# Kernel tuning notes

Measured on AMD Instinct MI355X. Metric: run time of the kernel, lower is better.

The kernel has to match this reference:

```python
import jax, jax.numpy as jnp
import numpy as np

RSQRT2 = 2 ** (-0.5)
B, S, D_IN = 2, 4096, 1024
H, D_HEAD = 8, 64            # num_heads, attention_dim (per-head qk and v dim)
QK_DIM = H * D_HEAD          # 512
V_DIM = H * D_HEAD           # 512
OUT_DIM = D_IN               # 1024 (output_dim defaults to input_dim)
LN_EPS = 1e-5


def setup_inputs() -> dict:
    key = jax.random.key(0)
    ks = jax.random.split(key, 8)
    def lecun(k, fan_in, shape):
        return jax.random.normal(k, shape, dtype=jnp.float32) * (1.0 / np.sqrt(fan_in))
    return {
        "x": jax.random.normal(ks[0], (B, S, D_IN), dtype=jnp.float32),
        # weights stored [in, out] (transposed torch Linear layout)
        "W_qk": lecun(ks[1], D_IN, (D_IN, 2 * QK_DIM)),
        "b_qk": jnp.zeros((2 * QK_DIM,), jnp.float32),
        "W_v": lecun(ks[2], D_IN, (D_IN, V_DIM)),
        "b_v": jnp.zeros((V_DIM,), jnp.float32),
        "W_out": lecun(ks[3], V_DIM, (V_DIM, OUT_DIM)),
        "b_out": jnp.zeros((OUT_DIM,), jnp.float32),
        "ln_gamma": jnp.ones((OUT_DIM,), jnp.float32),
        "ln_beta": jnp.zeros((OUT_DIM,), jnp.float32),
    }


def _layernorm(y, gamma, beta):
    mu = jnp.mean(y, axis=-1, keepdims=True)
    var = jnp.mean(jnp.square(y - mu), axis=-1, keepdims=True)
    return (y - mu) * jax.lax.rsqrt(var + LN_EPS) * gamma + beta


def reference(x, W_qk, b_qk, W_v, b_v, W_out, b_out, ln_gamma, ln_beta):
    b, s, _ = x.shape
    scale = D_HEAD ** (-0.5)
    qk = x @ W_qk + b_qk                          # [b, s, 2*h*d]
    qk = qk.reshape(b, s, H, D_HEAD, 2)           # c (q/k) is fastest axis
    q, k = qk[..., 0], qk[..., 1]                 # [b, s, h, d]
    v = (x @ W_v + b_v).reshape(b, s, H, D_HEAD)  # [b, s, h, d]
    # manual multi-head attention, full O(s^2) score matrix (as in source)
    sim = jnp.einsum("bihd,bjhd->bhij", q, k) * scale
    attn = jax.nn.softmax(sim, axis=-1)           # [b, h, i, j]
    o = jnp.einsum("bhij,bjhd->bihd", attn, v)    # [b, s, h, d]
    o = o.reshape(b, s, V_DIM)                    # 'b h s d -> b s (h d)'
    y = _layernorm(o @ W_out + b_out, ln_gamma, ln_beta)
    return (y + x) * RSQRT2
```

## Files before the change

### kernel.cpp

```cpp
#include <hip/hip_runtime.h>
#include <stdint.h>

typedef short bf16x8 __attribute__((ext_vector_type(8)));
typedef float f32x4 __attribute__((ext_vector_type(4)));
typedef unsigned short ushort_t;

#define RSQRT2_F 0.70710678118654752440f
#define QSCALE_F 0.18033688011114382f

__device__ __forceinline__ ushort_t f2bf(float f) {
  union { float f; uint32_t u; } c; c.f = f;
  uint32_t u = c.u;
  uint32_t r = (u + 0x7fffu + ((u >> 16) & 1u)) >> 16;
  return (ushort_t)r;
}
__device__ __forceinline__ float bf2f(ushort_t u) {
  union { uint32_t u; float f; } c; c.u = ((uint32_t)u) << 16;
  return c.f;
}
__device__ __forceinline__ uint32_t fbits(float f) {
  union { float f; uint32_t u; } c; c.f = f; return c.u;
}

__device__ __forceinline__ void gload_lds16(const void* g, void* l) {
  __builtin_amdgcn_global_load_lds(
      (const __attribute__((address_space(1))) void*)g,
      (__attribute__((address_space(3))) void*)l, 16, 0, 0);
}

__global__ __launch_bounds__(256) void k_cvt_x(const float* __restrict__ x,
                                               ushort_t* __restrict__ xb) {
  int i = (blockIdx.x * 256 + threadIdx.x) * 4;
  float4 f = *(const float4*)(x + i);
  ushort4 o;
  o.x = f2bf(f.x); o.y = f2bf(f.y); o.z = f2bf(f.z); o.w = f2bf(f.w);
  *(ushort4*)(xb + i) = o;
}

__global__ __launch_bounds__(256) void k_build_wqkv(const float* __restrict__ Wqk,
                                                    const float* __restrict__ bqk,
                                                    const float* __restrict__ Wv,
                                                    const float* __restrict__ bv,
                                                    ushort_t* __restrict__ Wt,
                                                    float* __restrict__ biasAll) {
  int k = blockIdx.x * 256 + threadIdx.x;
  int n = blockIdx.y;
  float w, bb;
  if (n < 512)       { w = Wqk[(size_t)k * 1024 + 2 * n] * QSCALE_F;     bb = bqk[2 * n] * QSCALE_F; }
  else if (n < 1024) { w = Wqk[(size_t)k * 1024 + 2 * (n - 512) + 1];    bb = bqk[2 * (n - 512) + 1]; }
  else               { w = Wv[(size_t)k * 512 + (n - 1024)];             bb = bv[n - 1024]; }
  Wt[(size_t)n * 1024 + k] = f2bf(w);
  if (k == 0) biasAll[n] = bb;
}

__global__ __launch_bounds__(256) void k_build_wout(const float* __restrict__ Wout,
                                                    ushort_t* __restrict__ Wt) {
  int k = blockIdx.x * 256 + threadIdx.x;
  int n = blockIdx.y;
  Wt[(size_t)n * 512 + k] = f2bf(Wout[(size_t)k * 1024 + n]);
}

template <int MODE>
__global__ __launch_bounds__(256) void k_gemm_bt(
    const ushort_t* __restrict__ A, const ushort_t* __restrict__ Bt,
    const float* __restrict__ bias,
    ushort_t* __restrict__ out0, ushort_t* __restrict__ out1, ushort_t* __restrict__ out2,
    int M, int N, int K) {
  __shared__ __align__(16) ushort_t As[4][128][8];
  __shared__ __align__(16) ushort_t Bs[4][128][8];
  const int t = threadIdx.x;
  const int lane = t & 63;
  const int wave = t >> 6;
  const int m0 = blockIdx.x * 128, n0 = blockIdx.y * 128;
  const int wm = (wave >> 1) * 64, wn = (wave & 1) * 64;
  const int lg = lane >> 4, lr = lane & 15;

  const int srow = t & 127, sg = t >> 7;
  ushort_t* lA0 = &As[sg][srow][0];
  ushort_t* lA1 = &As[sg + 2][srow][0];
  ushort_t* lB0 = &Bs[sg][srow][0];
  ushort_t* lB1 = &Bs[sg + 2][srow][0];
  const ushort_t* gA = A + (size_t)(m0 + srow) * K + sg * 8;
  const ushort_t* gB = Bt + (size_t)(n0 + srow) * K + sg * 8;

  f32x4 acc[4][4] = {};

  for (int k0 = 0; k0 < K; k0 += 32) {
    __syncthreads();
    gload_lds16(gA + k0, lA0);
    gload_lds16(gA + k0 + 16, lA1);
    gload_lds16(gB + k0, lB0);
    gload_lds16(gB + k0 + 16, lB1);
    __syncthreads();
    bf16x8 af[4], bfr[4];
#pragma unroll
    for (int mi = 0; mi < 4; mi++) af[mi] = *(const bf16x8*)&As[lg][wm + mi * 16 + lr][0];
#pragma unroll
    for (int ni = 0; ni < 4; ni++) bfr[ni] = *(const bf16x8*)&Bs[lg][wn + ni * 16 + lr][0];
#pragma unroll
    for (int mi = 0; mi < 4; mi++)
#pragma unroll
      for (int ni = 0; ni < 4; ni++)
        acc[mi][ni] = __builtin_amdgcn_mfma_f32_16x16x32_bf16(af[mi], bfr[ni], acc[mi][ni], 0, 0, 0);
  }

#pragma unroll
  for (int mi = 0; mi < 4; mi++) {
    int rowb = m0 + wm + mi * 16 + (lane >> 4) * 4;
#pragma unroll
    for (int ni = 0; ni < 4; ni++) {
      int col = n0 + wn + ni * 16 + lr;
      float bc = bias[col];
#pragma unroll
      for (int reg = 0; reg < 4; reg++) {
        int row = rowb + reg;
        float v = acc[mi][ni][reg] + bc;
        if (MODE == 0) {
          if (col < 512) {
            out0[(size_t)row * 512 + col] = f2bf(v);
          } else if (col < 1024) {
            out1[(size_t)row * 512 + (col - 512)] = f2bf(v);
          } else {
            int hd = col - 1024;
            int bb = row >> 12, s = row & 4095;
            out2[((size_t)(bb << 9) + hd) * 4096 + s] = f2bf(v);
          }
        } else {
          out0[(size_t)row * 1024 + col] = f2bf(v);
        }
      }
    }
  }
}

__global__ __launch_bounds__(256, 2) void k_attn(const ushort_t* __restrict__ Qb,
                                                 const ushort_t* __restrict__ Kb,
                                                 const ushort_t* __restrict__ Vt,
                                                 ushort_t* __restrict__ O0,
                                                 ushort_t* __restrict__ O1,
                                                 float* __restrict__ lpart) {
  __shared__ __align__(16) ushort_t Ks[2][8][64][8];
  __shared__ __align__(16) ushort_t Vs[2][8][64][8];
  __shared__ __align__(16) ushort_t Pl[4][1024];
  const int S = 4096;
  const int t = threadIdx.x, lane = t & 63, wave = t >> 6;
  const int lg = lane >> 4, lr = lane & 15;

  const int bid = blockIdx.x;
  const int xcd = bid & 7, idx = bid >> 3;
  const int bh = (xcd << 1) | (idx >> 5);
  const int rem = idx & 31;
  const int qb = rem >> 1;
  const int half = rem & 1;
  const int b = bh >> 3, h = bh & 7;
  const int qbase = qb * 256 + wave * 64;
  const int kvbase = half * 2048;

  bf16x8 qf[4][2];
#pragma unroll
  for (int su = 0; su < 4; su++) {
    const ushort_t* qp = Qb + ((size_t)(b * S + qbase + su * 16 + lr)) * 512 + h * 64 + lg * 8;
    qf[su][0] = *(const bf16x8*)qp;
    qf[su][1] = *(const bf16x8*)(qp + 32);
  }

  const int cj = t & 63, cg = t >> 6;
  const ushort_t* gK = Kb + ((size_t)b * S + cj) * 512 + h * 64 + cg * 8;
  const ushort_t* gV = Vt + ((size_t)bh * 64 + cj) * 4096 + cg * 8;

  const bf16x8 vones = {(short)0x3F80, (short)0x3F80, (short)0x3F80, (short)0x3F80,
                        (short)0x3F80, (short)0x3F80, (short)0x3F80, (short)0x3F80};

  int poff[4], pread[2];
#pragma unroll
  for (int nt = 0; nt < 4; nt++) poff[nt] = (lr * 128 + nt * 32 + lg * 8) ^ ((lr & 7) << 4);
#pragma unroll
  for (int kc = 0; kc < 2; kc++) pread[kc] = (lr * 128 + kc * 64 + lg * 16) ^ ((lr & 7) << 4);

  f32x4 of[4][4] = {};
  f32x4 of_sum[4] = {};

#define ATTN_STAGE(kv0, bsel)                                         \
  do {                                                                \
    gload_lds16(gK + (size_t)(kv0) * 512, &Ks[bsel][cg][cj][0]);      \
    gload_lds16(gK + (size_t)(kv0) * 512 + 32, &Ks[bsel][cg + 4][cj][0]); \
    gload_lds16(gV + (kv0), &Vs[bsel][cg][cj][0]);                    \
    gload_lds16(gV + (kv0) + 32, &Vs[bsel][cg + 4][cj][0]);           \
  } while (0)

  ATTN_STAGE(kvbase, 0);
  __syncthreads();
  int buf = 0;

  for (int kv0 = kvbase; kv0 < kvbase + 2048; kv0 += 64) {
    if (kv0 + 64 < kvbase + 2048) ATTN_STAGE(kv0 + 64, buf ^ 1);

    f32x4 sf[4][4];
    __builtin_amdgcn_s_setprio(1);
#pragma unroll
    for (int nt = 0; nt < 4; nt++) {
      bf16x8 kf0 = *(const bf16x8*)&Ks[buf][lg][nt * 16 + lr][0];
      bf16x8 kf1 = *(const bf16x8*)&Ks[buf][4 + lg][nt * 16 + lr][0];
#pragma unroll
      for (int su = 0; su < 4; su++) {
        f32x4 z = {};
        z = __builtin_amdgcn_mfma_f32_16x16x32_bf16(kf0, qf[su][0], z, 0, 0, 0);
        sf[su][nt] = __builtin_amdgcn_mfma_f32_16x16x32_bf16(kf1, qf[su][1], z, 0, 0, 0);
      }
    }
    __builtin_amdgcn_s_setprio(0);

    bf16x8 pf[4][2];
#pragma unroll
    for (int su = 0; su < 4; su++) {
      char* Pb = (char*)&Pl[wave][0];
#pragma unroll
      for (int nt = 0; nt < 4; nt++) {
        float p0 = __builtin_amdgcn_exp2f(sf[su][nt][0]);
        float p1 = __builtin_amdgcn_exp2f(sf[su][nt][1]);
        float p2 = __builtin_amdgcn_exp2f(sf[su][nt][2]);
        float p3 = __builtin_amdgcn_exp2f(sf[su][nt][3]);
        uint32_t w0 = (fbits(p0) >> 16) | (fbits(p1) & 0xffff0000u);
        uint32_t w1 = (fbits(p2) >> 16) | (fbits(p3) & 0xffff0000u);
        *(uint2*)(Pb + poff[nt]) = make_uint2(w0, w1);
      }
#pragma unroll
      for (int kc = 0; kc < 2; kc++) pf[su][kc] = *(const bf16x8*)(Pb + pread[kc]);
    }

    __builtin_amdgcn_s_setprio(1);
#pragma unroll
    for (int dt = 0; dt < 4; dt++) {
      bf16x8 vf0 = *(const bf16x8*)&Vs[buf][lg][dt * 16 + lr][0];
      bf16x8 vf1 = *(const bf16x8*)&Vs[buf][4 + lg][dt * 16 + lr][0];
#pragma unroll
      for (int su = 0; su < 4; su++) {
        of[su][dt] = __builtin_amdgcn_mfma_f32_16x16x32_bf16(pf[su][0], vf0, of[su][dt], 0, 0, 0);
        of[su][dt] = __builtin_amdgcn_mfma_f32_16x16x32_bf16(pf[su][1], vf1, of[su][dt], 0, 0, 0);
      }
    }
#pragma unroll
    for (int su = 0; su < 4; su++) {
      of_sum[su] = __builtin_amdgcn_mfma_f32_16x16x32_bf16(pf[su][0], vones, of_sum[su], 0, 0, 0);
      of_sum[su] = __builtin_amdgcn_mfma_f32_16x16x32_bf16(pf[su][1], vones, of_sum[su], 0, 0, 0);
    }
    __builtin_amdgcn_s_setprio(0);

    __syncthreads();
    buf ^= 1;
  }
#undef ATTN_STAGE

  ushort_t* Opw = (half ? O1 : O0) + (size_t)b * 4096 * 512;
#pragma unroll
  for (int su = 0; su < 4; su++) {
#pragma unroll
    for (int dt = 0; dt < 4; dt++)
#pragma unroll
      for (int r = 0; r < 4; r++) {
        int q = qbase + su * 16 + lg * 4 + r;
        Opw[(size_t)q * 512 + h * 64 + dt * 16 + lr] = f2bf(of[su][dt][r]);
      }
    if (lr == 0) {
#pragma unroll
      for (int r = 0; r < 4; r++) {
        int q = qbase + su * 16 + lg * 4 + r;
        lpart[(((size_t)half * 2 + b) * 8 + h) * 4096 + q] = of_sum[su][r];
      }
    }
  }
}

__global__ __launch_bounds__(128) void k_merge(const ushort_t* __restrict__ O0,
                                               const ushort_t* __restrict__ O1,
                                               const float* __restrict__ lpart,
                                               ushort_t* __restrict__ Ob) {
  const int row = blockIdx.x;
  const int t = threadIdx.x;
  const int col = t * 4;
  const int b = row >> 12, q = row & 4095;
  const int h = col >> 6;
  float l = lpart[(((size_t)0 * 2 + b) * 8 + h) * 4096 + q] +
            lpart[(((size_t)1 * 2 + b) * 8 + h) * 4096 + q];
  float inv = 1.0f / l;
  ushort4 a0 = *(const ushort4*)(O0 + (size_t)row * 512 + col);
  ushort4 a1 = *(const ushort4*)(O1 + (size_t)row * 512 + col);
  ushort4 o;
  o.x = f2bf((bf2f(a0.x) + bf2f(a1.x)) * inv);
  o.y = f2bf((bf2f(a0.y) + bf2f(a1.y)) * inv);
  o.z = f2bf((bf2f(a0.z) + bf2f(a1.z)) * inv);
  o.w = f2bf((bf2f(a0.w) + bf2f(a1.w)) * inv);
  *(ushort4*)(Ob + (size_t)row * 512 + col) = o;
}

__global__ __launch_bounds__(256) void k_ln(const ushort_t* __restrict__ ypre,
                                            const float* __restrict__ x,
                                            const float* __restrict__ gamma,
                                            const float* __restrict__ beta,
                                            float* __restrict__ out) {
  __shared__ float red[8];
  const int row = blockIdx.x, t = threadIdx.x;
  const ushort_t* yr = ypre + (size_t)row * 1024;
  ushort4 u = *(const ushort4*)(yr + t * 4);
  float v0 = bf2f(u.x), v1 = bf2f(u.y), v2 = bf2f(u.z), v3 = bf2f(u.w);
  float s = v0 + v1 + v2 + v3;
  float sq = v0 * v0 + v1 * v1 + v2 * v2 + v3 * v3;
#pragma unroll
  for (int m = 32; m; m >>= 1) { s += __shfl_xor(s, m, 64); sq += __shfl_xor(sq, m, 64); }
  if ((t & 63) == 0) { red[t >> 6] = s; red[4 + (t >> 6)] = sq; }
  __syncthreads();
  s = red[0] + red[1] + red[2] + red[3];
  sq = red[4] + red[5] + red[6] + red[7];
  float mu = s * (1.f / 1024.f);
  float var = sq * (1.f / 1024.f) - mu * mu;
  float inv = rsqrtf(var + 1e-5f);
  int c = t * 4;
  float4 xf = *(const float4*)(x + (size_t)row * 1024 + c);
  float4 o;
  o.x = ((v0 - mu) * inv * gamma[c + 0] + beta[c + 0] + xf.x) * RSQRT2_F;
  o.y = ((v1 - mu) * inv * gamma[c + 1] + beta[c + 1] + xf.y) * RSQRT2_F;
  o.z = ((v2 - mu) * inv * gamma[c + 2] + beta[c + 2] + xf.z) * RSQRT2_F;
  o.w = ((v3 - mu) * inv * gamma[c + 3] + beta[c + 3] + xf.w) * RSQRT2_F;
  *(float4*)(out + (size_t)row * 1024 + c) = o;
}

extern "C" void kernel_launch(void* const* d_in, const int* in_sizes, int n_in,
                              void* d_out, int out_size, void* d_ws, size_t ws_size,
                              hipStream_t stream) {
  (void)in_sizes; (void)n_in; (void)out_size; (void)ws_size;
  const float* x     = (const float*)d_in[0];
  const float* Wqk   = (const float*)d_in[1];
  const float* bqk   = (const float*)d_in[2];
  const float* Wv    = (const float*)d_in[3];
  const float* bv    = (const float*)d_in[4];
  const float* Wout  = (const float*)d_in[5];
  const float* bout  = (const float*)d_in[6];
  const float* gamma = (const float*)d_in[7];
  const float* beta  = (const float*)d_in[8];
  float* out = (float*)d_out;

  char* ws = (char*)d_ws;
  size_t off = 0;
  auto alloc = [&](size_t bytes) {
    off = (off + 255) & ~(size_t)255;
    void* p = ws + off;
    off += bytes;
    return p;
  };
  ushort_t* xb    = (ushort_t*)alloc(8192ull * 1024 * 2);
  ushort_t* Wqkvt = (ushort_t*)alloc(1536ull * 1024 * 2);
  float*    biasA = (float*)   alloc(1536ull * 4);
  ushort_t* Woutt = (ushort_t*)alloc(1024ull * 512 * 2);
  ushort_t* Qb    = (ushort_t*)alloc(8192ull * 512 * 2);
  ushort_t* Kbuf  = (ushort_t*)alloc(8192ull * 512 * 2);
  ushort_t* Vtb   = (ushort_t*)alloc(1024ull * 4096 * 2);
  float*    lpart = (float*)   alloc(2ull * 2 * 8 * 4096 * 4);
  ushort_t* O0    = xb;
  ushort_t* O1    = xb + 8192ull * 512;
  ushort_t* Obm   = Qb;
  ushort_t* ypre  = xb;

  k_cvt_x<<<8192, 256, 0, stream>>>(x, xb);
  k_build_wqkv<<<dim3(4, 1536), 256, 0, stream>>>(Wqk, bqk, Wv, bv, Wqkvt, biasA);
  k_build_wout<<<dim3(2, 1024), 256, 0, stream>>>(Wout, Woutt);
  k_gemm_bt<0><<<dim3(64, 12), 256, 0, stream>>>(xb, Wqkvt, biasA, Qb, Kbuf, Vtb, 8192, 1536, 1024);
  k_attn<<<512, 256, 0, stream>>>(Qb, Kbuf, Vtb, O0, O1, lpart);
  k_merge<<<8192, 128, 0, stream>>>(O0, O1, lpart, Obm);
  k_gemm_bt<1><<<dim3(64, 8), 256, 0, stream>>>(Obm, Woutt, bout, ypre, nullptr, nullptr, 8192, 1024, 512);
  k_ln<<<8192, 256, 0, stream>>>(ypre, x, gamma, beta, out);
}
```

Measured before the change: 203.2 us.

## Load K/V fragments directly from global memory and compute row sums on VALU

```diff
diff --git a/kernel.cpp b/kernel.cpp
--- a/kernel.cpp
+++ b/kernel.cpp
@@ -139,8 +139,6 @@
                                                  ushort_t* __restrict__ O0,
                                                  ushort_t* __restrict__ O1,
                                                  float* __restrict__ lpart) {
-  __shared__ __align__(16) ushort_t Ks[2][8][64][8];
-  __shared__ __align__(16) ushort_t Vs[2][8][64][8];
   __shared__ __align__(16) ushort_t Pl[4][1024];
   const int S = 4096;
   const int t = threadIdx.x, lane = t & 63, wave = t >> 6;
@@ -164,92 +162,75 @@
     qf[su][1] = *(const bf16x8*)(qp + 32);
   }
 
-  const int cj = t & 63, cg = t >> 6;
-  const ushort_t* gK = Kb + ((size_t)b * S + cj) * 512 + h * 64 + cg * 8;
-  const ushort_t* gV = Vt + ((size_t)bh * 64 + cj) * 4096 + cg * 8;
-
-  const bf16x8 vones = {(short)0x3F80, (short)0x3F80, (short)0x3F80, (short)0x3F80,
-                        (short)0x3F80, (short)0x3F80, (short)0x3F80, (short)0x3F80};
+  const ushort_t* Kbase = Kb + (size_t)(b * S) * 512 + h * 64 + lg * 8;
+  const ushort_t* Vbase = Vt + ((size_t)(bh * 64) + lr) * 4096 + lg * 8;
 
   int poff[4], pread[2];
 #pragma unroll
   for (int nt = 0; nt < 4; nt++) poff[nt] = (lr * 128 + nt * 32 + lg * 8) ^ ((lr & 7) << 4);
 #pragma unroll
   for (int kc = 0; kc < 2; kc++) pread[kc] = (lr * 128 + kc * 64 + lg * 16) ^ ((lr & 7) << 4);
+  char* Pb = (char*)&Pl[wave][0];
 
   f32x4 of[4][4] = {};
-  f32x4 of_sum[4] = {};
-
-#define ATTN_STAGE(kv0, bsel)                                         \
-  do {                                                                \
-    gload_lds16(gK + (size_t)(kv0) * 512, &Ks[bsel][cg][cj][0]);      \
-    gload_lds16(gK + (size_t)(kv0) * 512 + 32, &Ks[bsel][cg + 4][cj][0]); \
-    gload_lds16(gV + (kv0), &Vs[bsel][cg][cj][0]);                    \
-    gload_lds16(gV + (kv0) + 32, &Vs[bsel][cg + 4][cj][0]);           \
-  } while (0)
-
-  ATTN_STAGE(kvbase, 0);
-  __syncthreads();
-  int buf = 0;
+  float psum[4] = {0.f, 0.f, 0.f, 0.f};
 
   for (int kv0 = kvbase; kv0 < kvbase + 2048; kv0 += 64) {
-    if (kv0 + 64 < kvbase + 2048) ATTN_STAGE(kv0 + 64, buf ^ 1);
-
-    f32x4 sf[4][4];
-    __builtin_amdgcn_s_setprio(1);
+    bf16x8 kf[4][2], vf[4][2];
 #pragma unroll
     for (int nt = 0; nt < 4; nt++) {
-      bf16x8 kf0 = *(const bf16x8*)&Ks[buf][lg][nt * 16 + lr][0];
-      bf16x8 kf1 = *(const bf16x8*)&Ks[buf][4 + lg][nt * 16 + lr][0];
-#pragma unroll
-      for (int su = 0; su < 4; su++) {
+      const ushort_t* kp = Kbase + (size_t)(kv0 + nt * 16 + lr) * 512;
+      kf[nt][0] = *(const bf16x8*)kp;
+      kf[nt][1] = *(const bf16x8*)(kp + 32);
+    }
+#pragma unroll
+    for (int dt = 0; dt < 4; dt++) {
+      const ushort_t* vp = Vbase + (size_t)dt * (16 * 4096) + kv0;
+      vf[dt][0] = *(const bf16x8*)vp;
+      vf[dt][1] = *(const bf16x8*)(vp + 32);
+    }
+
+#pragma unroll
+    for (int su = 0; su < 4; su++) {
+      f32x4 sf[4];
+      __builtin_amdgcn_s_setprio(1);
+#pragma unroll
+      for (int nt = 0; nt < 4; nt++) {
         f32x4 z = {};
-        z = __builtin_amdgcn_mfma_f32_16x16x32_bf16(kf0, qf[su][0], z, 0, 0, 0);
-        sf[su][nt] = __builtin_amdgcn_mfma_f32_16x16x32_bf16(kf1, qf[su][1], z, 0, 0, 0);
-      }
-    }
-    __builtin_amdgcn_s_setprio(0);
-
-    bf16x8 pf[4][2];
-#pragma unroll
-    for (int su = 0; su < 4; su++) {
-      char* Pb = (char*)&Pl[wave][0];
+        z = __builtin_amdgcn_mfma_f32_16x16x32_bf16(kf[nt][0], qf[su][0], z, 0, 0, 0);
+        sf[nt] = __builtin_amdgcn_mfma_f32_16x16x32_bf16(kf[nt][1], qf[su][1], z, 0, 0, 0);
+      }
+      __builtin_amdgcn_s_setprio(0);
+
 #pragma unroll
       for (int nt = 0; nt < 4; nt++) {
-        float p0 = __builtin_amdgcn_exp2f(sf[su][nt][0]);
-        float p1 = __builtin_amdgcn_exp2f(sf[su][nt][1]);
-        float p2 = __builtin_amdgcn_exp2f(sf[su][nt][2]);
-        float p3 = __builtin_amdgcn_exp2f(sf[su][nt][3]);
+        float p0 = __builtin_amdgcn_exp2f(sf[nt][0]);
+        float p1 = __builtin_amdgcn_exp2f(sf[nt][1]);
+        float p2 = __builtin_amdgcn_exp2f(sf[nt][2]);
+        float p3 = __builtin_amdgcn_exp2f(sf[nt][3]);
+        psum[su] += (p0 + p1) + (p2 + p3);
         uint32_t w0 = (fbits(p0) >> 16) | (fbits(p1) & 0xffff0000u);
         uint32_t w1 = (fbits(p2) >> 16) | (fbits(p3) & 0xffff0000u);
         *(uint2*)(Pb + poff[nt]) = make_uint2(w0, w1);
       }
-#pragma unroll
-      for (int kc = 0; kc < 2; kc++) pf[su][kc] = *(const bf16x8*)(Pb + pread[kc]);
-    }
-
-    __builtin_amdgcn_s_setprio(1);
-#pragma unroll
-    for (int dt = 0; dt < 4; dt++) {
-      bf16x8 vf0 = *(const bf16x8*)&Vs[buf][lg][dt * 16 + lr][0];
-      bf16x8 vf1 = *(const bf16x8*)&Vs[buf][4 + lg][dt * 16 + lr][0];
-#pragma unroll
-      for (int su = 0; su < 4; su++) {
-        of[su][dt] = __builtin_amdgcn_mfma_f32_16x16x32_bf16(pf[su][0], vf0, of[su][dt], 0, 0, 0);
-        of[su][dt] = __builtin_amdgcn_mfma_f32_16x16x32_bf16(pf[su][1], vf1, of[su][dt], 0, 0, 0);
-      }
-    }
-#pragma unroll
-    for (int su = 0; su < 4; su++) {
-      of_sum[su] = __builtin_amdgcn_mfma_f32_16x16x32_bf16(pf[su][0], vones, of_sum[su], 0, 0, 0);
-      of_sum[su] = __builtin_amdgcn_mfma_f32_16x16x32_bf16(pf[su][1], vones, of_sum[su], 0, 0, 0);
-    }
-    __builtin_amdgcn_s_setprio(0);
-
-    __syncthreads();
-    buf ^= 1;
-  }
-#undef ATTN_STAGE
+      bf16x8 pf0 = *(const bf16x8*)(Pb + pread[0]);
+      bf16x8 pf1 = *(const bf16x8*)(Pb + pread[1]);
+
+      __builtin_amdgcn_s_setprio(1);
+#pragma unroll
+      for (int dt = 0; dt < 4; dt++) {
+        of[su][dt] = __builtin_amdgcn_mfma_f32_16x16x32_bf16(pf0, vf[dt][0], of[su][dt], 0, 0, 0);
+        of[su][dt] = __builtin_amdgcn_mfma_f32_16x16x32_bf16(pf1, vf[dt][1], of[su][dt], 0, 0, 0);
+      }
+      __builtin_amdgcn_s_setprio(0);
+    }
+  }
+
+#pragma unroll
+  for (int su = 0; su < 4; su++) {
+    psum[su] += __shfl_xor(psum[su], 16, 64);
+    psum[su] += __shfl_xor(psum[su], 32, 64);
+  }
 
   ushort_t* Opw = (half ? O1 : O0) + (size_t)b * 4096 * 512;
 #pragma unroll
@@ -261,12 +242,9 @@
         int q = qbase + su * 16 + lg * 4 + r;
         Opw[(size_t)q * 512 + h * 64 + dt * 16 + lr] = f2bf(of[su][dt][r]);
       }
-    if (lr == 0) {
-#pragma unroll
-      for (int r = 0; r < 4; r++) {
-        int q = qbase + su * 16 + lg * 4 + r;
-        lpart[(((size_t)half * 2 + b) * 8 + h) * 4096 + q] = of_sum[su][r];
-      }
+    if (lg == 0) {
+      int q = qbase + su * 16 + lr;
+      lpart[(((size_t)half * 2 + b) * 8 + h) * 4096 + q] = psum[su];
     }
   }
 }
```

Result: slower. 249.5 us (+22.8%).
